# Kernel optimization log

Hardware: AMD Instinct MI355X
Metric: run time of the kernel (lower is better)

The kernel has to match this reference:

```python
import jax, jax.numpy as jnp
import numpy as np

NUM_HEADS = 8
HEAD_DIM = 96  # dim_out // num_heads = 768 // 8
DIM_OUT = 768
STRIDE = 2


def setup_inputs() -> dict:
    key = jax.random.key(0)
    k1, k2, k3, k4, k5 = jax.random.split(key, 5)
    B, H, W, C = 4, 64, 64, 384
    hidden_states = jax.random.normal(k1, (B, H, W, C), dtype=jnp.float32)
    qkv_w = jax.random.normal(k2, (C, 3 * DIM_OUT), dtype=jnp.float32) * (C ** -0.5)
    qkv_b = jax.random.normal(k3, (3 * DIM_OUT,), dtype=jnp.float32) * 0.02
    proj_w = jax.random.normal(k4, (DIM_OUT, DIM_OUT), dtype=jnp.float32) * (DIM_OUT ** -0.5)
    proj_b = jax.random.normal(k5, (DIM_OUT,), dtype=jnp.float32) * 0.02
    return {"hidden_states": hidden_states, "qkv_w": qkv_w, "qkv_b": qkv_b,
            "proj_w": proj_w, "proj_b": proj_b}


def reference(hidden_states, qkv_w, qkv_b, proj_w, proj_b):
    B, H, W, C = hidden_states.shape
    scale = HEAD_DIM ** -0.5
    # QKV projection over channels
    qkv = jnp.einsum('bhwc,cd->bhwd', hidden_states, qkv_w) + qkv_b  # [B,H,W,3*Do]
    qkv = qkv.reshape(B, H * W, 3, NUM_HEADS, HEAD_DIM)
    q, k, v = qkv[:, :, 0], qkv[:, :, 1], qkv[:, :, 2]  # [B, HW, nh, hd]
    # Max-pool queries spatially by STRIDE
    q = q.reshape(B, H, W, DIM_OUT)
    Hq, Wq = H // STRIDE, W // STRIDE
    q = q.reshape(B, Hq, STRIDE, Wq, STRIDE, DIM_OUT).max(axis=(2, 4))  # [B,Hq,Wq,Do]
    q = q.reshape(B, Hq * Wq, NUM_HEADS, HEAD_DIM)
    # Attention: Lq = Hq*Wq, Lk = H*W
    attn = jnp.einsum('bqhd,bkhd->bhqk', q * scale, k)
    attn = jax.nn.softmax(attn, axis=-1)
    out = jnp.einsum('bhqk,bkhd->bqhd', attn, v)  # [B,Lq,nh,hd]
    out = out.reshape(B, Hq, Wq, DIM_OUT)
    out = jnp.einsum('bhwc,cd->bhwd', out, proj_w) + proj_b
    return out
```

## Files before the change

### kernel.cpp

```cpp
#include <hip/hip_runtime.h>
#include <hip/hip_bf16.h>

typedef unsigned short u16;
typedef __attribute__((ext_vector_type(8))) short bf16x8;
typedef __attribute__((ext_vector_type(8))) unsigned short u16x8;
typedef __attribute__((ext_vector_type(4))) float f32x4;

#define MFMA16(a,b,c) __builtin_amdgcn_mfma_f32_16x16x32_bf16(a,b,c,0,0,0)

__device__ __forceinline__ u16 f2bf(float f) {
  union { float f; unsigned int u; } v; v.f = f;
  unsigned int r = v.u + 0x7fffu + ((v.u >> 16) & 1u);
  return (u16)(r >> 16);
}
__device__ __forceinline__ float bf2f(u16 u) {
  union { unsigned int i; float f; } v; v.i = ((unsigned int)u) << 16; return v.f;
}
__device__ __forceinline__ float exp2a(float x) {
  float r;
  asm("v_exp_f32 %0, %1" : "=v"(r) : "v"(x));
  return r;
}
__device__ __forceinline__ float max3(float a, float b, float c) {
  float r;
  asm("v_max3_f32 %0, %1, %2, %3" : "=v"(r) : "v"(a), "v"(b), "v"(c));
  return r;
}

__device__ __forceinline__ void gld16(const void* g, void* l) {
  __builtin_amdgcn_global_load_lds((const __attribute__((address_space(1))) void*)g,
                                   (__attribute__((address_space(3))) void*)l, 16, 0, 0);
}

__device__ __forceinline__ void ttrans_body(const float* __restrict__ in, u16* __restrict__ out,
                                            int K, int N, int blk, int tid, u16 T[64][65]) {
  const int ntx = N >> 6;
  const int tx = blk % ntx, ty = blk / ntx;
  const int n0 = tx * 64, k0 = ty * 64;
  #pragma unroll
  for (int p = 0; p < 4; ++p) {
    int idx = p * 256 + tid;
    int r = idx >> 4, ch = idx & 15;
    float4 v = *reinterpret_cast<const float4*>(in + (size_t)(k0 + r) * N + n0 + ch * 4);
    T[r][ch * 4 + 0] = f2bf(v.x);
    T[r][ch * 4 + 1] = f2bf(v.y);
    T[r][ch * 4 + 2] = f2bf(v.z);
    T[r][ch * 4 + 3] = f2bf(v.w);
  }
  __syncthreads();
  #pragma unroll
  for (int p = 0; p < 2; ++p) {
    int idx = p * 256 + tid;
    int rr = idx >> 3, ch = idx & 7;
    u16x8 o;
    #pragma unroll
    for (int e = 0; e < 8; ++e) o[e] = T[ch * 8 + e][rr];
    *reinterpret_cast<u16x8*>(out + (size_t)(n0 + rr) * K + k0 + ch * 8) = o;
  }
}

__global__ void prep(const float* __restrict__ hs, u16* __restrict__ hs_bf,
                     const float* __restrict__ qkv_w, u16* __restrict__ qkvwT,
                     const float* __restrict__ proj_w, u16* __restrict__ projwT) {
  __shared__ u16 T[64][65];
  const int blk = blockIdx.x, tid = threadIdx.x;
  if (blk < 6144) {
    int i = blk * 256 + tid;
    float4 v = reinterpret_cast<const float4*>(hs)[i];
    ushort4 o; o.x = f2bf(v.x); o.y = f2bf(v.y); o.z = f2bf(v.z); o.w = f2bf(v.w);
    reinterpret_cast<ushort4*>(hs_bf)[i] = o;
  } else if (blk < 6360) {
    ttrans_body(qkv_w, qkvwT, 384, 2304, blk - 6144, tid, T);
  } else {
    ttrans_body(proj_w, projwT, 768, 768, blk - 6360, tid, T);
  }
}

template<int EPI>
__launch_bounds__(256)
__global__ void gemm_bt(const u16* __restrict__ A, const u16* __restrict__ Bt,
                        const float* __restrict__ bias,
                        u16* __restrict__ qp, u16* __restrict__ ok, u16* __restrict__ ov,
                        float* __restrict__ of, int K, int nbx, int cpx) {
  __shared__ __align__(16) u16 Sh[16384];
  const int id = blockIdx.x;
  const int id2 = (id & 7) * cpx + (id >> 3);
  const int bx = id2 % nbx, by = id2 / nbx;
  const int tid = threadIdx.x;
  const int wave = tid >> 6, lane = tid & 63;
  const int c = lane & 15, g = lane >> 4;
  const int brow = by * 128, bcol = bx * 128;
  const int wr = (wave >> 1) * 64, wc = (wave & 1) * 64;
  f32x4 acc[4][4] = {};
  const int srow = wave * 32 + (lane >> 2);
  const int scol = (lane & 3) * 8;
  const u16* agp0 = A  + (size_t)(brow + srow) * K + scol;
  const u16* agp1 = A  + (size_t)(brow + srow + 16) * K + scol;
  const u16* bgp0 = Bt + (size_t)(bcol + srow) * K + scol;
  const u16* bgp1 = Bt + (size_t)(bcol + srow + 16) * K + scol;
  const int lo0 = wave * 1024, lo1 = wave * 1024 + 512;
  const int nk = K >> 5;
  gld16(agp0, &Sh[lo0]);
  gld16(agp1, &Sh[lo1]);
  gld16(bgp0, &Sh[8192 + lo0]);
  gld16(bgp1, &Sh[8192 + lo1]);
  for (int ks = 0; ks < nk; ++ks) {
    const int cur = ks & 1;
    if (ks + 1 < nk) {
      const int k1 = (ks + 1) << 5;
      const int nb = (cur ^ 1) * 4096;
      gld16(agp0 + k1, &Sh[nb + lo0]);
      gld16(agp1 + k1, &Sh[nb + lo1]);
      gld16(bgp0 + k1, &Sh[8192 + nb + lo0]);
      gld16(bgp1 + k1, &Sh[8192 + nb + lo1]);
      asm volatile("s_waitcnt vmcnt(4)" ::: "memory");
    } else {
      asm volatile("s_waitcnt vmcnt(0)" ::: "memory");
    }
    __builtin_amdgcn_s_barrier();
    __builtin_amdgcn_sched_barrier(0);
    const int cb = cur * 4096;
    bf16x8 af[4], bfr[4];
    #pragma unroll
    for (int mi = 0; mi < 4; ++mi)
      af[mi] = *reinterpret_cast<const bf16x8*>(&Sh[cb + (wr + mi * 16 + c) * 32 + g * 8]);
    #pragma unroll
    for (int ni = 0; ni < 4; ++ni)
      bfr[ni] = *reinterpret_cast<const bf16x8*>(&Sh[8192 + cb + (wc + ni * 16 + c) * 32 + g * 8]);
    #pragma unroll
    for (int mi = 0; mi < 4; ++mi)
      #pragma unroll
      for (int ni = 0; ni < 4; ++ni)
        acc[mi][ni] = MFMA16(af[mi], bfr[ni], acc[mi][ni]);
    __builtin_amdgcn_sched_barrier(0);
    __builtin_amdgcn_s_barrier();
  }
  if (EPI == 0 && bcol < 768) {
    const float SC = 0.14724744f;
    float* P = (float*)&Sh[0];
    float m01[4][4], m23[4][4];
    #pragma unroll
    for (int mi = 0; mi < 4; ++mi)
      #pragma unroll
      for (int ni = 0; ni < 4; ++ni) {
        m01[mi][ni] = fmaxf(acc[mi][ni][0], acc[mi][ni][1]);
        m23[mi][ni] = fmaxf(acc[mi][ni][2], acc[mi][ni][3]);
      }
    if (wr == 64) {
      #pragma unroll
      for (int mi = 0; mi < 4; ++mi)
        #pragma unroll
        for (int ni = 0; ni < 4; ++ni) {
          const int pw = mi * 8 + g * 2;
          P[(wave & 1) * 2048 + pw * 64 + ni * 16 + c]       = m01[mi][ni];
          P[(wave & 1) * 2048 + (pw + 1) * 64 + ni * 16 + c] = m23[mi][ni];
        }
    }
    __syncthreads();
    if (wr == 0) {
      const int b = brow >> 12;
      const int hq = (brow >> 7) & 31;
      const size_t rbase = (size_t)(b * 1024 + hq * 32);
      #pragma unroll
      for (int mi = 0; mi < 4; ++mi)
        #pragma unroll
        for (int ni = 0; ni < 4; ++ni) {
          const int col = bcol + wc + ni * 16 + c;
          const float bz = bias[col];
          const int pw = mi * 8 + g * 2;
          float v0 = fmaxf(m01[mi][ni], P[(wave & 1) * 2048 + pw * 64 + ni * 16 + c]);
          float v1 = fmaxf(m23[mi][ni], P[(wave & 1) * 2048 + (pw + 1) * 64 + ni * 16 + c]);
          qp[(rbase + pw) * 768 + col]     = f2bf((v0 + bz) * SC);
          qp[(rbase + pw + 1) * 768 + col] = f2bf((v1 + bz) * SC);
        }
    }
    return;
  }
  if (EPI == 0 && bcol >= 1536) {
    u16* T = &Sh[0];
    const int vc0 = bcol - 1536;
    const int bq = brow >> 12;
    const int s0 = brow & 4095;
    #pragma unroll
    for (int ni = 0; ni < 4; ++ni) {
      const int j = wc + ni * 16 + c;
      const float bz = bias[bcol + j];
      const int key = (j & 15) << 2;
      #pragma unroll
      for (int mi = 0; mi < 4; ++mi) {
        const int rb = wr + mi * 16 + g * 4;
        ushort4 o;
        o.x = f2bf(acc[mi][ni][0] + bz);
        o.y = f2bf(acc[mi][ni][1] + bz);
        o.z = f2bf(acc[mi][ni][2] + bz);
        o.w = f2bf(acc[mi][ni][3] + bz);
        *reinterpret_cast<ushort4*>(&T[j * 128 + (rb ^ key)]) = o;
      }
    }
    __syncthreads();
    u16* vb2 = ov + ((size_t)(bq * 768 + vc0)) * 4096 + s0;
    #pragma unroll
    for (int p = 0; p < 8; ++p) {
      const int j = p * 16 + wave * 4 + (lane >> 4);
      const int sc = lane & 15;
      const int key = j & 15;
      const int p4 = 8 * (sc >> 3) + 2 * (sc & 3) + ((sc >> 2) & 1);
      uint2 lo = *reinterpret_cast<uint2*>(&T[j * 128 + ((sc ^ key) << 2)]);
      uint2 hi = *reinterpret_cast<uint2*>(&T[j * 128 + (((sc + 16) ^ key) << 2)]);
      *reinterpret_cast<uint2*>(vb2 + (size_t)j * 4096 + p4 * 4)      = lo;
      *reinterpret_cast<uint2*>(vb2 + (size_t)j * 4096 + 64 + p4 * 4) = hi;
    }
    return;
  }
  #pragma unroll
  for (int mi = 0; mi < 4; ++mi) {
    #pragma unroll
    for (int ni = 0; ni < 4; ++ni) {
      const int col = bcol + wc + ni * 16 + c;
      const float bz = bias[col];
      #pragma unroll
      for (int i = 0; i < 4; ++i) {
        const int row = brow + wr + mi * 16 + g * 4 + i;
        float v = acc[mi][ni][i] + bz;
        if (EPI == 0) {
          ok[(size_t)row * 768 + col - 768] = f2bf(v);
        } else {
          of[(size_t)row * 768 + col] = v;
        }
      }
    }
  }
}

__launch_bounds__(512, 4)
__global__ void flash8(const u16* __restrict__ Qp, const u16* __restrict__ Kb,
                       const u16* __restrict__ Vtg, u16* __restrict__ aout) {
  const int blk = blockIdx.x;
  const int xcd = blk & 7, j = blk >> 3;
  const int bh = xcd + 8 * (j >> 4), qt = j & 15;
  const int b = bh >> 3, h = bh & 7;
  __shared__ __align__(16) u16 Sh[24576];
  const int tid = threadIdx.x, w = tid >> 6, lane = tid & 63;
  const int sq = w >> 2, wq = w & 3;
  const int c = lane & 15, g = lane >> 4;
  const int kbase = sq * 12288;
  const int vbase = 6144 + sq * 12288;
  const u16* qb = Qp + ((size_t)(b * 1024 + qt * 64 + wq * 16 + c)) * 768 + h * 96;
  bf16x8 qf[3];
  #pragma unroll
  for (int kc = 0; kc < 3; ++kc)
    qf[kc] = *reinterpret_cast<const bf16x8*>(qb + kc * 32 + g * 8);
  const u16* kp[3];
  const u16* vp[3];
  int loff[3];
  {
    const u16* kb0 = Kb + ((size_t)(b * 4096 + sq * 2048)) * 768 + h * 96;
    const u16* vb0 = Vtg + ((size_t)(bh * 96)) * 4096 + sq * 2048;
    #pragma unroll
    for (int j2 = 0; j2 < 3; ++j2) {
      int p = wq * 192 + j2 * 64 + lane;
      int r = p / 12, ch = p - r * 12;
      kp[j2] = kb0 + r * 768 + ch * 8;
      int d = p >> 3, vch = p & 7;
      vp[j2] = vb0 + d * 4096 + ((vch ^ (d & 7)) * 8);
      loff[j2] = (wq * 192 + j2 * 64) * 8;
    }
  }
  float m = -1e30f, l = 0.f;
  f32x4 acc[6] = {};
  const f32x4 z4 = {0.f, 0.f, 0.f, 0.f};
  const int sw = (c & 7) << 3;
  for (int kt = 0; kt < 32; ++kt) {
    __syncthreads();
    #pragma unroll
    for (int j2 = 0; j2 < 3; ++j2) gld16(kp[j2], &Sh[kbase + loff[j2]]);
    #pragma unroll
    for (int j2 = 0; j2 < 3; ++j2) gld16(vp[j2], &Sh[vbase + loff[j2]]);
    #pragma unroll
    for (int j2 = 0; j2 < 3; ++j2) { kp[j2] += 49152; vp[j2] += 64; }
    __syncthreads();
    f32x4 st[4];
    __builtin_amdgcn_s_setprio(1);
    #pragma unroll
    for (int kt4 = 0; kt4 < 4; ++kt4) {
      bf16x8 kf = *reinterpret_cast<const bf16x8*>(&Sh[kbase + (kt4 * 16 + c) * 96 + g * 8]);
      st[kt4] = MFMA16(kf, qf[0], z4);
    }
    #pragma unroll
    for (int kc = 1; kc < 3; ++kc)
      #pragma unroll
      for (int kt4 = 0; kt4 < 4; ++kt4) {
        bf16x8 kf = *reinterpret_cast<const bf16x8*>(&Sh[kbase + (kt4 * 16 + c) * 96 + kc * 32 + g * 8]);
        st[kt4] = MFMA16(kf, qf[kc], st[kt4]);
      }
    __builtin_amdgcn_s_setprio(0);
    float pmax;
    {
      float a0 = max3(st[0][0], st[0][1], st[0][2]);
      float a1 = max3(st[0][3], st[1][0], st[1][1]);
      float a2 = max3(st[1][2], st[1][3], st[2][0]);
      float a3 = max3(st[2][1], st[2][2], st[2][3]);
      float a4 = max3(st[3][0], st[3][1], st[3][2]);
      pmax = fmaxf(max3(a0, a1, st[3][3]), max3(a2, a3, a4));
    }
    pmax = fmaxf(pmax, __shfl_xor(pmax, 16));
    pmax = fmaxf(pmax, __shfl_xor(pmax, 32));
    if (__any(pmax > m + 8.0f)) {
      float mn = fmaxf(m, pmax);
      float esc = exp2a(m - mn);
      m = mn;
      l *= esc;
      float er[4];
      #pragma unroll
      for (int i = 0; i < 4; ++i) er[i] = __shfl(esc, g * 4 + i);
      #pragma unroll
      for (int dc = 0; dc < 6; ++dc)
        #pragma unroll
        for (int i = 0; i < 4; ++i)
          acc[dc][i] *= er[i];
    }
    float ps = 0.f;
    #pragma unroll
    for (int kt4 = 0; kt4 < 4; ++kt4)
      #pragma unroll
      for (int i = 0; i < 4; ++i) {
        float p = exp2a(st[kt4][i] - m);
        st[kt4][i] = p;
        ps += p;
      }
    ps += __shfl_xor(ps, 16);
    ps += __shfl_xor(ps, 32);
    l += ps;
    unsigned int uu[4][2];
    #pragma unroll
    for (int kt4 = 0; kt4 < 4; ++kt4) {
      asm("v_cvt_pk_bf16_f32 %0, %1, %2" : "=v"(uu[kt4][0]) : "v"(st[kt4][0]), "v"(st[kt4][1]));
      asm("v_cvt_pk_bf16_f32 %0, %1, %2" : "=v"(uu[kt4][1]) : "v"(st[kt4][2]), "v"(st[kt4][3]));
    }
    __builtin_amdgcn_s_setprio(1);
    #pragma unroll
    for (int kh = 0; kh < 2; ++kh) {
      union { unsigned int wrd[4]; bf16x8 v; } pfu;
      pfu.wrd[0] = uu[2 * kh][0];
      pfu.wrd[1] = uu[2 * kh][1];
      pfu.wrd[2] = uu[2 * kh + 1][0];
      pfu.wrd[3] = uu[2 * kh + 1][1];
      bf16x8 pf = pfu.v;
      #pragma unroll
      for (int dc = 0; dc < 6; ++dc) {
        bf16x8 vf = *reinterpret_cast<const bf16x8*>(&Sh[vbase + (dc * 16 + c) * 64 + ((kh * 32 + g * 8) ^ sw)]);
        acc[dc] = MFMA16(pf, vf, acc[dc]);
      }
    }
    __builtin_amdgcn_s_setprio(0);
  }
  __syncthreads();
  float* Cb = (float*)&Sh[0];
  float* Ml = (float*)&Sh[12288];
  if (sq == 1) {
    #pragma unroll
    for (int dc = 0; dc < 6; ++dc)
      #pragma unroll
      for (int i = 0; i < 4; ++i)
        Cb[(wq * 16 + g * 4 + i) * 96 + dc * 16 + c] = acc[dc][i];
    if (lane < 16) {
      Ml[(wq * 16 + lane) * 2]     = m;
      Ml[(wq * 16 + lane) * 2 + 1] = l;
    }
  }
  __syncthreads();
  if (sq == 0) {
    u16* ob = aout + (size_t)(b * 1024 + qt * 64 + wq * 16) * 768 + h * 96;
    #pragma unroll
    for (int i = 0; i < 4; ++i) {
      const int q = g * 4 + i;
      float m0q = __shfl(m, q), l0q = __shfl(l, q);
      float m1q = Ml[(wq * 16 + q) * 2], l1q = Ml[(wq * 16 + q) * 2 + 1];
      float M = fmaxf(m0q, m1q);
      float e0 = exp2a(m0q - M), e1 = exp2a(m1q - M);
      float inv = 1.f / (l0q * e0 + l1q * e1);
      #pragma unroll
      for (int dc = 0; dc < 6; ++dc) {
        float a1 = Cb[(wq * 16 + q) * 96 + dc * 16 + c];
        ob[(size_t)q * 768 + dc * 16 + c] = f2bf((acc[dc][i] * e0 + a1 * e1) * inv);
      }
    }
  }
}

extern "C" void kernel_launch(void* const* d_in, const int* in_sizes, int n_in,
                              void* d_out, int out_size, void* d_ws, size_t ws_size,
                              hipStream_t stream) {
  const float* hs     = (const float*)d_in[0];
  const float* qkv_w  = (const float*)d_in[1];
  const float* qkv_b  = (const float*)d_in[2];
  const float* proj_w = (const float*)d_in[3];
  const float* proj_b = (const float*)d_in[4];
  float* out = (float*)d_out;

  u16* hs_bf  = (u16*)d_ws;
  u16* qkvwT  = hs_bf  + 6291456;
  u16* projwT = qkvwT  + 884736;
  u16* vT     = projwT + 589824;
  u16* kbuf   = vT     + 12582912;
  u16* spare  = kbuf   + 12582912;
  u16* qpol   = spare  + 12582912;
  u16* aout   = qpol   + 3145728;

  prep<<<6504, 256, 0, stream>>>(hs, hs_bf, qkv_w, qkvwT, proj_w, projwT);

  gemm_bt<0><<<2304, 256, 0, stream>>>(hs_bf, qkvwT, qkv_b,
                                       qpol, kbuf, vT, nullptr, 384, 18, 288);
  flash8<<<512, 512, 0, stream>>>(qpol, kbuf, vT, aout);
  gemm_bt<1><<<192, 256, 0, stream>>>(aout, projwT, proj_b,
                                      nullptr, nullptr, nullptr, out, 768, 6, 24);
}
```

Baseline: 146.8 us.

## Prefetch next K/V tile into registers to overlap global loads with compute

The flash attention kernel now loads the next K/V tile from global memory into registers while the current tile is being processed. At the top of each iteration those registers are stored to LDS, replacing the direct global-to-LDS loads that previously stalled at a barrier. Raw s_barrier and explicit lgkmcnt waits replace __syncthreads so that outstanding global loads are not drained. The cost is extra VGPRs, which could lower occupancy under the 512x4 launch bounds, plus an extra LDS write pass.

```diff
diff --git a/kernel.cpp b/kernel.cpp
--- a/kernel.cpp
+++ b/kernel.cpp
@@ -233,7 +233,7 @@
 }
 
 __launch_bounds__(512, 4)
-__global__ void flash8(const u16* __restrict__ Qp, const u16* __restrict__ Kb,
+__global__ void flash9(const u16* __restrict__ Qp, const u16* __restrict__ Kb,
                        const u16* __restrict__ Vtg, u16* __restrict__ aout) {
   const int blk = blockIdx.x;
   const int xcd = blk & 7, j = blk >> 3;
@@ -252,7 +252,7 @@
     qf[kc] = *reinterpret_cast<const bf16x8*>(qb + kc * 32 + g * 8);
   const u16* kp[3];
   const u16* vp[3];
-  int loff[3];
+  int lws[3];
   {
     const u16* kb0 = Kb + ((size_t)(b * 4096 + sq * 2048)) * 768 + h * 96;
     const u16* vb0 = Vtg + ((size_t)(bh * 96)) * 4096 + sq * 2048;
@@ -263,22 +263,41 @@
       kp[j2] = kb0 + r * 768 + ch * 8;
       int d = p >> 3, vch = p & 7;
       vp[j2] = vb0 + d * 4096 + ((vch ^ (d & 7)) * 8);
-      loff[j2] = (wq * 192 + j2 * 64) * 8;
+      lws[j2] = p * 8;
     }
   }
   float m = -1e30f, l = 0.f;
   f32x4 acc[6] = {};
   const f32x4 z4 = {0.f, 0.f, 0.f, 0.f};
   const int sw = (c & 7) << 3;
+  uint4 kreg[3], vreg[3];
+  #pragma unroll
+  for (int j2 = 0; j2 < 3; ++j2) kreg[j2] = *reinterpret_cast<const uint4*>(kp[j2]);
+  #pragma unroll
+  for (int j2 = 0; j2 < 3; ++j2) vreg[j2] = *reinterpret_cast<const uint4*>(vp[j2]);
+  #pragma unroll
+  for (int j2 = 0; j2 < 3; ++j2) { kp[j2] += 49152; vp[j2] += 64; }
   for (int kt = 0; kt < 32; ++kt) {
-    __syncthreads();
-    #pragma unroll
-    for (int j2 = 0; j2 < 3; ++j2) gld16(kp[j2], &Sh[kbase + loff[j2]]);
-    #pragma unroll
-    for (int j2 = 0; j2 < 3; ++j2) gld16(vp[j2], &Sh[vbase + loff[j2]]);
-    #pragma unroll
-    for (int j2 = 0; j2 < 3; ++j2) { kp[j2] += 49152; vp[j2] += 64; }
-    __syncthreads();
+    __builtin_amdgcn_s_barrier();
+    __builtin_amdgcn_sched_barrier(0);
+    #pragma unroll
+    for (int j2 = 0; j2 < 3; ++j2)
+      *reinterpret_cast<uint4*>(&Sh[kbase + lws[j2]]) = kreg[j2];
+    #pragma unroll
+    for (int j2 = 0; j2 < 3; ++j2)
+      *reinterpret_cast<uint4*>(&Sh[vbase + lws[j2]]) = vreg[j2];
+    if (kt < 31) {
+      #pragma unroll
+      for (int j2 = 0; j2 < 3; ++j2) kreg[j2] = *reinterpret_cast<const uint4*>(kp[j2]);
+      #pragma unroll
+      for (int j2 = 0; j2 < 3; ++j2) vreg[j2] = *reinterpret_cast<const uint4*>(vp[j2]);
+      #pragma unroll
+      for (int j2 = 0; j2 < 3; ++j2) { kp[j2] += 49152; vp[j2] += 64; }
+    }
+    __builtin_amdgcn_sched_barrier(0);
+    asm volatile("s_waitcnt lgkmcnt(0)" ::: "memory");
+    __builtin_amdgcn_s_barrier();
+    __builtin_amdgcn_sched_barrier(0);
     f32x4 st[4];
     __builtin_amdgcn_s_setprio(1);
     #pragma unroll
@@ -353,6 +372,8 @@
       }
     }
     __builtin_amdgcn_s_setprio(0);
+    __builtin_amdgcn_sched_barrier(0);
+    asm volatile("s_waitcnt lgkmcnt(0)" ::: "memory");
   }
   __syncthreads();
   float* Cb = (float*)&Sh[0];
@@ -411,7 +432,7 @@
 
   gemm_bt<0><<<2304, 256, 0, stream>>>(hs_bf, qkvwT, qkv_b,
                                        qpol, kbuf, vT, nullptr, 384, 18, 288);
-  flash8<<<512, 512, 0, stream>>>(qpol, kbuf, vT, aout);
+  flash9<<<512, 512, 0, stream>>>(qpol, kbuf, vT, aout);
   gemm_bt<1><<<192, 256, 0, stream>>>(aout, projwT, proj_b,
                                       nullptr, nullptr, nullptr, out, 768, 6, 24);
 }
```

New measurement: 292.9 us. 1.99x slower.

## Prefetch next K/V tile into registers during attention compute

Applied to the files above, without the earlier changes.

Replaces the direct global-to-LDS loads in the flash attention loop with register-staged prefetching. The next K/V tile is loaded into registers while the current tile is computed, then written to LDS after the barrier. This hides global memory latency behind the MFMA work, at the cost of extra VGPRs and hand-placed barriers and waitcnts that could restrict scheduling.

```diff
diff --git a/kernel.cpp b/kernel.cpp
--- a/kernel.cpp
+++ b/kernel.cpp
@@ -233,8 +233,8 @@
 }
 
 __launch_bounds__(512, 4)
-__global__ void flash8(const u16* __restrict__ Qp, const u16* __restrict__ Kb,
-                       const u16* __restrict__ Vtg, u16* __restrict__ aout) {
+__global__ void flash10(const u16* __restrict__ Qp, const u16* __restrict__ Kb,
+                        const u16* __restrict__ Vtg, u16* __restrict__ aout) {
   const int blk = blockIdx.x;
   const int xcd = blk & 7, j = blk >> 3;
   const int bh = xcd + 8 * (j >> 4), qt = j & 15;
@@ -250,35 +250,56 @@
   #pragma unroll
   for (int kc = 0; kc < 3; ++kc)
     qf[kc] = *reinterpret_cast<const bf16x8*>(qb + kc * 32 + g * 8);
-  const u16* kp[3];
-  const u16* vp[3];
-  int loff[3];
+  const u16 *kp0, *kp1, *kp2, *vp0, *vp1, *vp2;
+  int lw0, lw1, lw2;
   {
     const u16* kb0 = Kb + ((size_t)(b * 4096 + sq * 2048)) * 768 + h * 96;
     const u16* vb0 = Vtg + ((size_t)(bh * 96)) * 4096 + sq * 2048;
-    #pragma unroll
-    for (int j2 = 0; j2 < 3; ++j2) {
-      int p = wq * 192 + j2 * 64 + lane;
-      int r = p / 12, ch = p - r * 12;
-      kp[j2] = kb0 + r * 768 + ch * 8;
-      int d = p >> 3, vch = p & 7;
-      vp[j2] = vb0 + d * 4096 + ((vch ^ (d & 7)) * 8);
-      loff[j2] = (wq * 192 + j2 * 64) * 8;
-    }
+    int p0 = wq * 192 + lane, p1 = p0 + 64, p2 = p0 + 128;
+    int r0 = p0 / 12, c0 = p0 - r0 * 12;
+    int r1 = p1 / 12, c1 = p1 - r1 * 12;
+    int r2 = p2 / 12, c2 = p2 - r2 * 12;
+    kp0 = kb0 + r0 * 768 + c0 * 8;
+    kp1 = kb0 + r1 * 768 + c1 * 8;
+    kp2 = kb0 + r2 * 768 + c2 * 8;
+    vp0 = vb0 + (p0 >> 3) * 4096 + (((p0 & 7) ^ ((p0 >> 3) & 7)) * 8);
+    vp1 = vb0 + (p1 >> 3) * 4096 + (((p1 & 7) ^ ((p1 >> 3) & 7)) * 8);
+    vp2 = vb0 + (p2 >> 3) * 4096 + (((p2 & 7) ^ ((p2 >> 3) & 7)) * 8);
+    lw0 = p0 * 8; lw1 = p1 * 8; lw2 = p2 * 8;
   }
   float m = -1e30f, l = 0.f;
   f32x4 acc[6] = {};
   const f32x4 z4 = {0.f, 0.f, 0.f, 0.f};
   const int sw = (c & 7) << 3;
+  uint4 kr0 = *reinterpret_cast<const uint4*>(kp0);
+  uint4 kr1 = *reinterpret_cast<const uint4*>(kp1);
+  uint4 kr2 = *reinterpret_cast<const uint4*>(kp2);
+  uint4 vr0 = *reinterpret_cast<const uint4*>(vp0);
+  uint4 vr1 = *reinterpret_cast<const uint4*>(vp1);
+  uint4 vr2 = *reinterpret_cast<const uint4*>(vp2);
+  kp0 += 49152; kp1 += 49152; kp2 += 49152;
+  vp0 += 64; vp1 += 64; vp2 += 64;
   for (int kt = 0; kt < 32; ++kt) {
-    __syncthreads();
-    #pragma unroll
-    for (int j2 = 0; j2 < 3; ++j2) gld16(kp[j2], &Sh[kbase + loff[j2]]);
-    #pragma unroll
-    for (int j2 = 0; j2 < 3; ++j2) gld16(vp[j2], &Sh[vbase + loff[j2]]);
-    #pragma unroll
-    for (int j2 = 0; j2 < 3; ++j2) { kp[j2] += 49152; vp[j2] += 64; }
-    __syncthreads();
+    __builtin_amdgcn_s_barrier();
+    __builtin_amdgcn_sched_barrier(0);
+    *reinterpret_cast<uint4*>(&Sh[kbase + lw0]) = kr0;
+    *reinterpret_cast<uint4*>(&Sh[kbase + lw1]) = kr1;
+    *reinterpret_cast<uint4*>(&Sh[kbase + lw2]) = kr2;
+    *reinterpret_cast<uint4*>(&Sh[vbase + lw0]) = vr0;
+    *reinterpret_cast<uint4*>(&Sh[vbase + lw1]) = vr1;
+    *reinterpret_cast<uint4*>(&Sh[vbase + lw2]) = vr2;
+    kr0 = *reinterpret_cast<const uint4*>(kp0);
+    kr1 = *reinterpret_cast<const uint4*>(kp1);
+    kr2 = *reinterpret_cast<const uint4*>(kp2);
+    vr0 = *reinterpret_cast<const uint4*>(vp0);
+    vr1 = *reinterpret_cast<const uint4*>(vp1);
+    vr2 = *reinterpret_cast<const uint4*>(vp2);
+    kp0 += 49152; kp1 += 49152; kp2 += 49152;
+    vp0 += 64; vp1 += 64; vp2 += 64;
+    __builtin_amdgcn_sched_barrier(0);
+    asm volatile("s_waitcnt lgkmcnt(0)" ::: "memory");
+    __builtin_amdgcn_s_barrier();
+    __builtin_amdgcn_sched_barrier(0);
     f32x4 st[4];
     __builtin_amdgcn_s_setprio(1);
     #pragma unroll
@@ -353,6 +374,8 @@
       }
     }
     __builtin_amdgcn_s_setprio(0);
+    __builtin_amdgcn_sched_barrier(0);
+    asm volatile("s_waitcnt lgkmcnt(0)" ::: "memory");
   }
   __syncthreads();
   float* Cb = (float*)&Sh[0];
@@ -411,7 +434,7 @@
 
   gemm_bt<0><<<2304, 256, 0, stream>>>(hs_bf, qkvwT, qkv_b,
                                        qpol, kbuf, vT, nullptr, 384, 18, 288);
-  flash8<<<512, 512, 0, stream>>>(qpol, kbuf, vT, aout);
+  flash10<<<512, 512, 0, stream>>>(qpol, kbuf, vT, aout);
   gemm_bt<1><<<192, 256, 0, stream>>>(aout, projwT, proj_b,
                                       nullptr, nullptr, nullptr, out, 768, 6, 24);
 }
```

Result: slower. 152.6 us (+3.9%).
